# Performance work log

Hardware: AMD Instinct MI355X
Metric: run time of the kernel (lower is better)

Reference implementation:

```python
import jax, jax.numpy as jnp
import numpy as np
from jax import lax

K = 3
K2 = K * K
EPS = 1e-5


def conv3x3(x, w, b=None):
    # x [B,C,H,W], w [O,C,3,3], padding=1, stride=1
    out = lax.conv_general_dilated(x, w, (1, 1), [(1, 1), (1, 1)],
                                   dimension_numbers=('NCHW', 'OIHW', 'NCHW'))
    if b is not None:
        out = out + b[None, :, None, None]
    return out


def deform_conv(x, w_off, b_off, w_mod, b_mod, w):
    # DCNv2-style deformable conv, k=3, stride=1, pad=1, dilation=1, no bias.
    B, C, H, W = x.shape
    O = w.shape[0]
    off = conv3x3(x, w_off, b_off).reshape(B, K2, 2, H, W)   # (dy,dx) per tap
    mod = 2.0 * jax.nn.sigmoid(conv3x3(x, w_mod, b_mod))      # [B,9,H,W]
    dy, dx = off[:, :, 0], off[:, :, 1]

    ky = (jnp.arange(K) - 1).astype(x.dtype)
    base_y = jnp.repeat(ky, K)   # [9]
    base_x = jnp.tile(ky, K)     # [9]
    ii = jnp.arange(H, dtype=x.dtype)[:, None]
    jj = jnp.arange(W, dtype=x.dtype)[None, :]
    py = ii[None, None] + base_y[None, :, None, None] + dy   # [B,9,H,W]
    px = jj[None, None] + base_x[None, :, None, None] + dx

    def sample(xb, pyb, pxb):
        # xb [C,H,W]; pyb/pxb [9,H,W] -> [C,9,H,W], bilinear w/ zero pad
        y0 = jnp.floor(pyb)
        x0 = jnp.floor(pxb)
        wy = pyb - y0
        wx = pxb - x0
        flat = xb.reshape(C, -1)
        acc = jnp.zeros((C, K2, H, W), xb.dtype)
        for yc, xc, wt in ((y0, x0, (1 - wy) * (1 - wx)),
                           (y0, x0 + 1, (1 - wy) * wx),
                           (y0 + 1, x0, wy * (1 - wx)),
                           (y0 + 1, x0 + 1, wy * wx)):
            yi = yc.astype(jnp.int32)
            xi = xc.astype(jnp.int32)
            valid = (yi >= 0) & (yi < H) & (xi >= 0) & (xi < W)
            idx = (jnp.clip(yi, 0, H - 1) * W + jnp.clip(xi, 0, W - 1)).reshape(-1)
            g = jnp.take(flat, idx, axis=1).reshape(C, K2, H, W)
            acc = acc + g * (wt * valid)[None]
        return acc

    patches = jax.vmap(sample)(x, py, px)          # [B,C,9,H,W]
    patches = patches * mod[:, None]               # modulated
    return jnp.einsum('bckhw,ock->bohw', patches, w.reshape(O, C, K2))


def bn_relu(x):
    # BatchNorm2d(affine=False), train-mode batch stats, biased variance
    mean = jnp.mean(x, axis=(0, 2, 3), keepdims=True)
    var = jnp.mean(jnp.square(x - mean), axis=(0, 2, 3), keepdims=True)
    return jax.nn.relu((x - mean) * lax.rsqrt(var + EPS))


def maxpool2(x):
    return lax.reduce_window(x, -jnp.inf, lax.max, (1, 1, 2, 2), (1, 1, 2, 2), 'VALID')


def setup_inputs() -> dict:
    key = jax.random.key(0)
    ks = jax.random.split(key, 11)
    B, Cin, Cout, H, W = 4, 64, 128, 128, 128
    std1 = 1.0 / np.sqrt(Cin * K2)
    std2 = 1.0 / np.sqrt(Cout * K2)
    return {
        'x': jax.random.normal(ks[0], (B, Cin, H, W), jnp.float32),
        'w_off1': jax.random.normal(ks[1], (2 * K2, Cin, K, K), jnp.float32) * 0.01,
        'b_off1': jax.random.normal(ks[2], (2 * K2,), jnp.float32) * 0.01,
        'w_mod1': jax.random.normal(ks[3], (K2, Cin, K, K), jnp.float32) * 0.01,
        'b_mod1': jnp.zeros((K2,), jnp.float32),
        'w1': jax.random.normal(ks[4], (Cout, Cin, K, K), jnp.float32) * std1,
        'w_off2': jax.random.normal(ks[5], (2 * K2, Cout, K, K), jnp.float32) * 0.01,
        'b_off2': jax.random.normal(ks[6], (2 * K2,), jnp.float32) * 0.01,
        'w_mod2': jax.random.normal(ks[7], (K2, Cout, K, K), jnp.float32) * 0.01,
        'b_mod2': jnp.zeros((K2,), jnp.float32),
        'w2': jax.random.normal(ks[8], (Cout, Cout, K, K), jnp.float32) * std2,
    }


def reference(x, w_off1, b_off1, w_mod1, b_mod1, w1,
              w_off2, b_off2, w_mod2, b_mod2, w2):
    h = bn_relu(deform_conv(x, w_off1, b_off1, w_mod1, b_mod1, w1))
    h = bn_relu(deform_conv(h, w_off2, b_off2, w_mod2, b_mod2, w2))
    return maxpool2(h)
```

## Files before the change

kernel.cpp:

```cpp
#include <hip/hip_runtime.h>
#include <math.h>

#define HH 128
#define WW 128
#define HWSZ 16384

typedef __attribute__((ext_vector_type(8))) _Float16 h8;
typedef __attribute__((ext_vector_type(2))) _Float16 h2;
typedef __attribute__((ext_vector_type(4))) float f32x4;
typedef __attribute__((ext_vector_type(2))) float f32x2;
typedef unsigned short ushort;

__device__ __forceinline__ ushort f2h(float f) {
    _Float16 h = (_Float16)f;
    ushort u;
    __builtin_memcpy(&u, &h, 2);
    return u;
}
__device__ __forceinline__ unsigned f2h2(float lo, float hi) {
    h2 r;
    r.x = (_Float16)lo;
    r.y = (_Float16)hi;
    unsigned u;
    __builtin_memcpy(&u, &r, 4);
    return u;
}
__device__ __forceinline__ f32x2 unpk_h2(unsigned u) {
    h2 h;
    __builtin_memcpy(&h, &u, 4);
    return (f32x2){(float)h.x, (float)h.y};
}

__global__ __launch_bounds__(256) void prep_weights(
    const float* __restrict__ w1, const float* __restrict__ w2,
    const float* __restrict__ w_off1, const float* __restrict__ w_mod1,
    const float* __restrict__ w_off2, const float* __restrict__ w_mod2,
    ushort* __restrict__ Wt1, ushort* __restrict__ Wt2,
    ushort* __restrict__ Wo1, ushort* __restrict__ Wo2) {
    int bid = blockIdx.x, tid = threadIdx.x;
    if (bid < 336) {
        int i = bid * 256 + tid;
        int o = i / 672, kq = i % 672;
        int k = kq / 72, c = kq % 72;
        float v = (k < 9 && c < 64) ? w1[(o * 64 + c) * 9 + k] : 0.f;
        Wt1[i] = f2h(v);
    } else if (bid < 960) {
        int i = (bid - 336) * 256 + tid;
        int o = i / 1248, kq = i % 1248;
        int k = kq / 136, c = kq % 136;
        float v = (k < 9 && c < 128) ? w2[(o * 128 + c) * 9 + k] : 0.f;
        Wt2[i] = f2h(v);
    } else if (bid < 1032) {
        int i = (bid - 960) * 256 + tid;
        int o = i / 576, kap = i % 576;
        int k = kap / 64, c = kap % 64;
        float v = 0.f;
        if (o < 18) v = w_off1[(o * 64 + c) * 9 + k];
        else if (o < 27) v = w_mod1[((o - 18) * 64 + c) * 9 + k];
        Wo1[i] = f2h(v);
    } else {
        int i = (bid - 1032) * 256 + tid;
        int o = i / 1152, kap = i % 1152;
        int k = kap / 128, c = kap % 128;
        float v = 0.f;
        if (o < 18) v = w_off2[(o * 128 + c) * 9 + k];
        else if (o < 27) v = w_mod2[((o - 18) * 128 + c) * 9 + k];
        Wo2[i] = f2h(v);
    }
}

template <int C>
__global__ __launch_bounds__(256) void nhwc_cvt(const float* __restrict__ xin,
                                                unsigned* __restrict__ xout) {
    __shared__ float tile[64][C + 1];
    const int m0 = blockIdx.x * 64;
    const int b = m0 >> 14;
    const int hw0 = m0 & 16383;
    const int t = threadIdx.x;
    const int pr = t & 63, cr = t >> 6;
#pragma unroll
    for (int it = 0; it < C / 4; ++it) {
        int c = it * 4 + cr;
        tile[pr][c] = xin[(((size_t)(b * C + c)) << 14) + hw0 + pr];
    }
    __syncthreads();
    constexpr int CH = C / 2;
#pragma unroll
    for (int it = 0; it < 64 * CH / 256; ++it) {
        int slot = it * 256 + t;
        int p = slot / CH, cc = slot % CH;
        xout[(size_t)(m0 + p) * CH + cc] =
            f2h2(tile[p][2 * cc], tile[p][2 * cc + 1]);
    }
}

__global__ __launch_bounds__(256) void bn_apply_ew(
    const unsigned* __restrict__ xin, const float* __restrict__ praw,
    unsigned* __restrict__ xout) {
    __shared__ float lstats[256];
    if (threadIdx.x < 128) {
        int c = threadIdx.x;
        float s = 0.f, q = 0.f;
#pragma unroll
        for (int r = 0; r < 8; ++r) {
            s += praw[r * 256 + c];
            q += praw[r * 256 + 128 + c];
        }
        float mean = s / 65536.f;
        float var = q / 65536.f - mean * mean;
        lstats[c] = mean;
        lstats[128 + c] = rsqrtf(var + 1e-5f);
    }
    __syncthreads();
    int i = blockIdx.x * 256 + threadIdx.x;
    uint4 v = ((const uint4*)xin)[i];
    int c0 = ((i * 4) & 63) * 2;
    unsigned ov[4];
    unsigned in[4] = {v.x, v.y, v.z, v.w};
#pragma unroll
    for (int d = 0; d < 4; ++d) {
        int c = c0 + 2 * d;
        f32x2 f = unpk_h2(in[d]);
        float a = fmaxf(0.f, (f.x - lstats[c]) * lstats[128 + c]);
        float b2 = fmaxf(0.f, (f.y - lstats[c + 1]) * lstats[128 + c + 1]);
        ov[d] = f2h2(a, b2);
    }
    ((uint4*)xout)[i] = uint4{ov[0], ov[1], ov[2], ov[3]};
}

template <int C>
__global__ __launch_bounds__(256) void offmod_nhwc(
    const ushort* __restrict__ xh, const ushort* __restrict__ wt,
    const float* __restrict__ b_off, const float* __restrict__ b_mod,
    float* __restrict__ dyb, float* __restrict__ dxb, float* __restrict__ mob,
    float* __restrict__ praw) {
    constexpr int K = C * 9;
    if (blockIdx.x < 8) praw[blockIdx.x * 256 + threadIdx.x] = 0.f;
    const int m0 = blockIdx.x * 64;
    const int b = m0 >> 14;
    const int hw0 = m0 & 16383;
    const int h = hw0 >> 7;
    const int w0 = hw0 & 127;
    const int tid = threadIdx.x;
    const int lane = tid & 63, wv = tid >> 6;
    const int n16 = lane & 15, quad = lane >> 4;
    const int p = wv * 16 + n16;
    const int w = w0 + p;

    int tbase[9];
    bool tval[9];
#pragma unroll
    for (int k = 0; k < 9; ++k) {
        int yy = h + k / 3 - 1, xx = w + k % 3 - 1;
        tval[k] = ((unsigned)yy < 128u) && ((unsigned)xx < 128u);
        int cy = min(max(yy, 0), 127), cx = min(max(xx, 0), 127);
        tbase[k] = ((b << 14) + (cy << 7) + cx) * C + quad * 8;
    }

    f32x4 acc[2];
    acc[0] = (f32x4){0.f, 0.f, 0.f, 0.f};
    acc[1] = (f32x4){0.f, 0.f, 0.f, 0.f};

    const ushort* b0p = wt + (size_t)n16 * K + quad * 8;
    const ushort* b1p = wt + (size_t)(16 + n16) * K + quad * 8;

#pragma unroll
    for (int s = 0; s < K / 32; ++s) {
        const int k = (s * 32) / C;
        const int c0 = (s * 32) % C;
        h8 a = {0, 0, 0, 0, 0, 0, 0, 0};
        if (tval[k]) a = *(const h8*)(xh + (size_t)tbase[k] + c0);
        const h8 bv0 = *(const h8*)(b0p + s * 32);
        const h8 bv1 = *(const h8*)(b1p + s * 32);
        acc[0] = __builtin_amdgcn_mfma_f32_16x16x32_f16(a, bv0, acc[0], 0, 0, 0);
        acc[1] = __builtin_amdgcn_mfma_f32_16x16x32_f16(a, bv1, acc[1], 0, 0, 0);
    }

    __shared__ float sm[32 * 65];
#pragma unroll
    for (int nt = 0; nt < 2; ++nt) {
        int n = nt * 16 + n16;
        int pb = wv * 16 + quad * 4;
#pragma unroll
        for (int r = 0; r < 4; ++r) sm[n * 65 + pb + r] = acc[nt][r];
    }
    __syncthreads();
    {
        int n = tid >> 3, i8 = tid & 7;
        if (n < 27) {
            const float* sp = sm + n * 65 + i8 * 8;
            int px = hw0 + i8 * 8;
            if (n < 18) {
                int k = n >> 1;
                float bias = b_off[n];
                float* dst =
                    ((n & 1) ? dxb : dyb) + (((size_t)(b * 9 + k)) << 14) + px;
#pragma unroll
                for (int j = 0; j < 8; j += 4) {
                    float4 v = make_float4(sp[j] + bias, sp[j + 1] + bias,
                                           sp[j + 2] + bias, sp[j + 3] + bias);
                    *(float4*)(dst + j) = v;
                }
            } else {
                float bias = b_mod[n - 18];
                float* dst = mob + (((size_t)(b * 9 + (n - 18))) << 14) + px;
#pragma unroll
                for (int j = 0; j < 8; j += 4) {
                    float4 v;
                    v.x = 2.f / (1.f + expf(-(sp[j] + bias)));
                    v.y = 2.f / (1.f + expf(-(sp[j + 1] + bias)));
                    v.z = 2.f / (1.f + expf(-(sp[j + 2] + bias)));
                    v.w = 2.f / (1.f + expf(-(sp[j + 3] + bias)));
                    *(float4*)(dst + j) = v;
                }
            }
        }
    }
}

template <int C>
__global__ __launch_bounds__(256, 4) void deform_mfma3(
    const ushort* __restrict__ xh, const float* __restrict__ dyb,
    const float* __restrict__ dxb, const float* __restrict__ mob,
    const ushort* __restrict__ wt, unsigned* __restrict__ xout,
    float* __restrict__ praw) {
    constexpr int PIX = 64;
    constexpr int NCH = C / 8;
    constexpr int NCC = C / 8;
    constexpr int NIT = PIX * NCC / 256;
    constexpr int HNIT = NIT / 2;
    constexpr int SH = (C / 32) / 2 > 0 ? (C / 32) / 2 : 1;
    constexpr int CPW = C + 8;
    constexpr int KP = ((9 * CPW + 31) / 32) * 32;
    constexpr int ABUF = PIX * C;
    constexpr int LOOPB = 2 * ABUF * 2 + PIX * 9 * 4 + PIX * 9 * 8;
    constexpr int EPIB = 128 * (PIX + 1) * 4;
    constexpr int SMEMB = LOOPB > EPIB ? LOOPB : EPIB;

    __shared__ __align__(16) char smem_raw[SMEMB];
    ushort* abuf0 = (ushort*)smem_raw;
    ushort* abuf1 = abuf0 + ABUF;
    int* tbl = (int*)(abuf0 + 2 * ABUF);
    unsigned* twl = (unsigned*)(smem_raw + 2 * ABUF * 2 + PIX * 9 * 4);

    const int bid = (blockIdx.x & 7) * (gridDim.x >> 3) + (blockIdx.x >> 3);
    const int m0 = bid * PIX;
    const int b = m0 >> 14;
    const int hw0 = m0 & 16383;
    const int h = hw0 >> 7, w0 = hw0 & 127;
    const int tid = threadIdx.x;
    const int lane = tid & 63, wv = tid >> 6;
    const int n16 = lane & 15, quad = lane >> 4;
    const int xr = n16 & (NCH - 1);

    for (int r = tid; r < PIX * 9; r += 256) {
        int p = r & (PIX - 1), k = r >> 6;
        int oi = ((b * 9 + k) << 14) + hw0 + p;
        float py = (float)(h + k / 3 - 1) + dyb[oi];
        float px = (float)(w0 + p + k % 3 - 1) + dxb[oi];
        float mv = mob[oi];
        float y0f = floorf(py), x0f = floorf(px);
        float wy = py - y0f, wx = px - x0f;
        int y0 = (int)y0f, x0 = (int)x0f;
        int y1 = y0 + 1, x1 = x0 + 1;
        float f00 = (1.f - wy) * (1.f - wx) *
                    (((unsigned)y0 < 128u && (unsigned)x0 < 128u) ? mv : 0.f);
        float f01 = (1.f - wy) * wx *
                    (((unsigned)y0 < 128u && (unsigned)x1 < 128u) ? mv : 0.f);
        float f10 = wy * (1.f - wx) *
                    (((unsigned)y1 < 128u && (unsigned)x0 < 128u) ? mv : 0.f);
        float f11 = wy * wx *
                    (((unsigned)y1 < 128u && (unsigned)x1 < 128u) ? mv : 0.f);
        int cy0 = min(max(y0, 0), 127), cy1 = min(max(y1, 0), 127);
        int cx0 = min(max(x0, 0), 127), cx1 = min(max(x1, 0), 127);
        int base00 = (((b << 14) + (cy0 << 7) + cx0)) * C;
        int flags = ((cy1 != cy0) ? 2 : 0) | ((cx1 != cx0) ? 1 : 0);
        int s = p * 9 + k;
        tbl[s] = base00 | flags;
        twl[2 * s] = f2h2(f00, f01);
        twl[2 * s + 1] = f2h2(f10, f11);
    }
    __syncthreads();

    auto issue_loads = [&](int kc, int it0, uint4 (&q)[HNIT][4],
                           uint2 (&fw)[HNIT]) {
#pragma unroll
        for (int j = 0; j < HNIT; ++j) {
            int e = (it0 + j) * 256 + tid;
            int p = e / NCC, cc = e % NCC;
            int s = p * 9 + kc;
            int ent = tbl[s];
            fw[j] = *(const uint2*)&twl[2 * s];
            int base = ent & ~3;
            int dxo = (ent & 1) ? C : 0;
            int dyo = (ent & 2) ? (C << 7) : 0;
            const ushort* pp = xh + (size_t)base + cc * 8;
            q[j][0] = *(const uint4*)(pp);
            q[j][1] = *(const uint4*)(pp + dxo);
            q[j][2] = *(const uint4*)(pp + dyo);
            q[j][3] = *(const uint4*)(pp + dyo + dxo);
        }
    };
    auto interp_write = [&](ushort* dst, int it0, uint4 (&q)[HNIT][4],
                            uint2 (&fw)[HNIT]) {
#pragma unroll
        for (int j = 0; j < HNIT; ++j) {
            int e = (it0 + j) * 256 + tid;
            int p = e / NCC, cc = e % NCC;
            h2 w01, w23;
            __builtin_memcpy(&w01, &fw[j].x, 4);
            __builtin_memcpy(&w23, &fw[j].y, 4);
            h8 F0 = {w01.x, w01.x, w01.x, w01.x, w01.x, w01.x, w01.x, w01.x};
            h8 F1 = {w01.y, w01.y, w01.y, w01.y, w01.y, w01.y, w01.y, w01.y};
            h8 F2 = {w23.x, w23.x, w23.x, w23.x, w23.x, w23.x, w23.x, w23.x};
            h8 F3 = {w23.y, w23.y, w23.y, w23.y, w23.y, w23.y, w23.y, w23.y};
            h8 a0, a1, a2, a3;
            __builtin_memcpy(&a0, &q[j][0], 16);
            __builtin_memcpy(&a1, &q[j][1], 16);
            __builtin_memcpy(&a2, &q[j][2], 16);
            __builtin_memcpy(&a3, &q[j][3], 16);
            h8 v = a0 * F0 + a1 * F1 + a2 * F2 + a3 * F3;
            uint4 ov;
            __builtin_memcpy(&ov, &v, 16);
            int ccs = cc ^ (p & (NCH - 1));
            *(uint4*)&dst[p * C + ccs * 8] = ov;
        }
    };

    f32x4 acc[4][2];
#pragma unroll
    for (int mt = 0; mt < 4; ++mt)
#pragma unroll
        for (int nt = 0; nt < 2; ++nt) acc[mt][nt] = (f32x4){0.f, 0.f, 0.f, 0.f};

    const ushort* bbase[2];
#pragma unroll
    for (int nt = 0; nt < 2; ++nt)
        bbase[nt] = wt + (size_t)(wv * 32 + nt * 16 + n16) * KP + quad * 8;

    auto mfma_run = [&](const ushort* ab, int kc, int s0, int s1) {
#pragma unroll
        for (int s = s0; s < s1; ++s) {
            h8 av[4], bv[2];
            int ch = (s * 4 + quad) ^ xr;
#pragma unroll
            for (int mt = 0; mt < 4; ++mt)
                av[mt] = *(const h8*)(ab + (mt * 16 + n16) * C + ch * 8);
#pragma unroll
            for (int nt = 0; nt < 2; ++nt)
                bv[nt] = *(const h8*)(bbase[nt] + kc * CPW + s * 32);
#pragma unroll
            for (int mt = 0; mt < 4; ++mt)
#pragma unroll
                for (int nt = 0; nt < 2; ++nt)
                    acc[mt][nt] = __builtin_amdgcn_mfma_f32_16x16x32_f16(
                        av[mt], bv[nt], acc[mt][nt], 0, 0, 0);
        }
    };

    {
        uint4 q[HNIT][4];
        uint2 fw[HNIT];
        issue_loads(0, 0, q, fw);
        interp_write(abuf0, 0, q, fw);
        issue_loads(0, HNIT, q, fw);
        interp_write(abuf0, HNIT, q, fw);
    }
    __syncthreads();

#pragma unroll 1
    for (int kc = 0; kc < 9; ++kc) {
        const ushort* ab = (kc & 1) ? abuf1 : abuf0;
        ushort* dst = (kc & 1) ? abuf0 : abuf1;
        uint4 q[HNIT][4];
        uint2 fw[HNIT];
        if (kc < 8) issue_loads(kc + 1, 0, q, fw);
        __builtin_amdgcn_s_setprio(1);
        mfma_run(ab, kc, 0, SH);
        __builtin_amdgcn_s_setprio(0);
        if (kc < 8) {
            interp_write(dst, 0, q, fw);
            issue_loads(kc + 1, HNIT, q, fw);
        }
        __builtin_amdgcn_s_setprio(1);
        mfma_run(ab, kc, SH, C / 32);
        __builtin_amdgcn_s_setprio(0);
        if (kc < 8) interp_write(dst, HNIT, q, fw);
        __syncthreads();
    }

    float* sm = (float*)smem_raw;
    constexpr int SROW = PIX + 1;
#pragma unroll
    for (int mt = 0; mt < 4; ++mt)
#pragma unroll
        for (int nt = 0; nt < 2; ++nt) {
            int o = wv * 32 + nt * 16 + n16;
            int mb = mt * 16 + quad * 4;
#pragma unroll
            for (int r = 0; r < 4; ++r) sm[o * SROW + mb + r] = acc[mt][nt][r];
        }
    __syncthreads();
    {
        int o = tid >> 1, half = tid & 1;
        const float* sp = sm + o * SROW + half * 32;
        float s = 0.f, qq = 0.f;
#pragma unroll
        for (int i = 0; i < 32; i += 4) {
            float4 v = make_float4(sp[i], sp[i + 1], sp[i + 2], sp[i + 3]);
            s += v.x + v.y + v.z + v.w;
            qq += v.x * v.x + v.y * v.y + v.z * v.z + v.w * v.w;
        }
        s += __shfl_down(s, 1, 64);
        qq += __shfl_down(qq, 1, 64);
        if (half == 0) {
            float* pr = praw + (blockIdx.x & 7) * 256;
            atomicAdd(&pr[o], s);
            atomicAdd(&pr[128 + o], qq);
        }
    }
    {
        int p = tid >> 2, cc4 = tid & 3;
        unsigned ov[16];
#pragma unroll
        for (int j = 0; j < 16; ++j) {
            int c = cc4 * 32 + 2 * j;
            ov[j] = f2h2(sm[c * SROW + p], sm[(c + 1) * SROW + p]);
        }
        uint4* dst = (uint4*)(xout + ((size_t)(m0 + p)) * 64 + cc4 * 16);
        dst[0] = uint4{ov[0], ov[1], ov[2], ov[3]};
        dst[1] = uint4{ov[4], ov[5], ov[6], ov[7]};
        dst[2] = uint4{ov[8], ov[9], ov[10], ov[11]};
        dst[3] = uint4{ov[12], ov[13], ov[14], ov[15]};
    }
}

template <int C>
__global__ __launch_bounds__(256, 4) void deform_mfma3p(
    const ushort* __restrict__ xh, const float* __restrict__ dyb,
    const float* __restrict__ dxb, const float* __restrict__ mob,
    const ushort* __restrict__ wt, float* __restrict__ pout,
    float* __restrict__ praw) {
    constexpr int PIX = 64;
    constexpr int NCH = C / 8;
    constexpr int NCC = C / 8;
    constexpr int NIT = PIX * NCC / 256;
    constexpr int HNIT = NIT / 2;
    constexpr int SH = (C / 32) / 2 > 0 ? (C / 32) / 2 : 1;
    constexpr int CPW = C + 8;
    constexpr int KP = ((9 * CPW + 31) / 32) * 32;
    constexpr int ABUF = PIX * C;
    constexpr int LOOPB = 2 * ABUF * 2 + PIX * 9 * 4 + PIX * 9 * 8;
    constexpr int EPIB = 128 * (PIX + 1) * 4;
    constexpr int SMEMB = LOOPB > EPIB ? LOOPB : EPIB;

    __shared__ __align__(16) char smem_raw[SMEMB];
    ushort* abuf0 = (ushort*)smem_raw;
    ushort* abuf1 = abuf0 + ABUF;
    int* tbl = (int*)(abuf0 + 2 * ABUF);
    unsigned* twl = (unsigned*)(smem_raw + 2 * ABUF * 2 + PIX * 9 * 4);

    const int bid = (blockIdx.x & 7) * (gridDim.x >> 3) + (blockIdx.x >> 3);
    const int b = bid >> 8;
    const int rp = (bid >> 2) & 63;
    const int g = bid & 3;
    const int tid = threadIdx.x;
    const int lane = tid & 63, wv = tid >> 6;
    const int n16 = lane & 15, quad = lane >> 4;
    const int xr = n16 & (NCH - 1);

    for (int r = tid; r < PIX * 9; r += 256) {
        int p = r & (PIX - 1), k = r >> 6;
        int row = 2 * rp + (p >> 5), col = g * 32 + (p & 31);
        int oi = ((b * 9 + k) << 14) + (row << 7) + col;
        float py = (float)(row + k / 3 - 1) + dyb[oi];
        float px = (float)(col + k % 3 - 1) + dxb[oi];
        float mv = mob[oi];
        float y0f = floorf(py), x0f = floorf(px);
        float wy = py - y0f, wx = px - x0f;
        int y0 = (int)y0f, x0 = (int)x0f;
        int y1 = y0 + 1, x1 = x0 + 1;
        float f00 = (1.f - wy) * (1.f - wx) *
                    (((unsigned)y0 < 128u && (unsigned)x0 < 128u) ? mv : 0.f);
        float f01 = (1.f - wy) * wx *
                    (((unsigned)y0 < 128u && (unsigned)x1 < 128u) ? mv : 0.f);
        float f10 = wy * (1.f - wx) *
                    (((unsigned)y1 < 128u && (unsigned)x0 < 128u) ? mv : 0.f);
        float f11 = wy * wx *
                    (((unsigned)y1 < 128u && (unsigned)x1 < 128u) ? mv : 0.f);
        int cy0 = min(max(y0, 0), 127), cy1 = min(max(y1, 0), 127);
        int cx0 = min(max(x0, 0), 127), cx1 = min(max(x1, 0), 127);
        int base00 = (((b << 14) + (cy0 << 7) + cx0)) * C;
        int flags = ((cy1 != cy0) ? 2 : 0) | ((cx1 != cx0) ? 1 : 0);
        int s = p * 9 + k;
        tbl[s] = base00 | flags;
        twl[2 * s] = f2h2(f00, f01);
        twl[2 * s + 1] = f2h2(f10, f11);
    }
    __syncthreads();

    auto issue_loads = [&](int kc, int it0, uint4 (&q)[HNIT][4],
                           uint2 (&fw)[HNIT]) {
#pragma unroll
        for (int j = 0; j < HNIT; ++j) {
            int e = (it0 + j) * 256 + tid;
            int p = e / NCC, cc = e % NCC;
            int s = p * 9 + kc;
            int ent = tbl[s];
            fw[j] = *(const uint2*)&twl[2 * s];
            int base = ent & ~3;
            int dxo = (ent & 1) ? C : 0;
            int dyo = (ent & 2) ? (C << 7) : 0;
            const ushort* pp = xh + (size_t)base + cc * 8;
            q[j][0] = *(const uint4*)(pp);
            q[j][1] = *(const uint4*)(pp + dxo);
            q[j][2] = *(const uint4*)(pp + dyo);
            q[j][3] = *(const uint4*)(pp + dyo + dxo);
        }
    };
    auto interp_write = [&](ushort* dst, int it0, uint4 (&q)[HNIT][4],
                            uint2 (&fw)[HNIT]) {
#pragma unroll
        for (int j = 0; j < HNIT; ++j) {
            int e = (it0 + j) * 256 + tid;
            int p = e / NCC, cc = e % NCC;
            h2 w01, w23;
            __builtin_memcpy(&w01, &fw[j].x, 4);
            __builtin_memcpy(&w23, &fw[j].y, 4);
            h8 F0 = {w01.x, w01.x, w01.x, w01.x, w01.x, w01.x, w01.x, w01.x};
            h8 F1 = {w01.y, w01.y, w01.y, w01.y, w01.y, w01.y, w01.y, w01.y};
            h8 F2 = {w23.x, w23.x, w23.x, w23.x, w23.x, w23.x, w23.x, w23.x};
            h8 F3 = {w23.y, w23.y, w23.y, w23.y, w23.y, w23.y, w23.y, w23.y};
            h8 a0, a1, a2, a3;
            __builtin_memcpy(&a0, &q[j][0], 16);
            __builtin_memcpy(&a1, &q[j][1], 16);
            __builtin_memcpy(&a2, &q[j][2], 16);
            __builtin_memcpy(&a3, &q[j][3], 16);
            h8 v = a0 * F0 + a1 * F1 + a2 * F2 + a3 * F3;
            uint4 ov;
            __builtin_memcpy(&ov, &v, 16);
            int ccs = cc ^ (p & (NCH - 1));
            *(uint4*)&dst[p * C + ccs * 8] = ov;
        }
    };

    f32x4 acc[4][2];
#pragma unroll
    for (int mt = 0; mt < 4; ++mt)
#pragma unroll
        for (int nt = 0; nt < 2; ++nt) acc[mt][nt] = (f32x4){0.f, 0.f, 0.f, 0.f};

    const ushort* bbase[2];
#pragma unroll
    for (int nt = 0; nt < 2; ++nt)
        bbase[nt] = wt + (size_t)(wv * 32 + nt * 16 + n16) * KP + quad * 8;

    auto mfma_run = [&](const ushort* ab, int kc, int s0, int s1) {
#pragma unroll
        for (int s = s0; s < s1; ++s) {
            h8 av[4], bv[2];
            int ch = (s * 4 + quad) ^ xr;
#pragma unroll
            for (int mt = 0; mt < 4; ++mt)
                av[mt] = *(const h8*)(ab + (mt * 16 + n16) * C + ch * 8);
#pragma unroll
            for (int nt = 0; nt < 2; ++nt)
                bv[nt] = *(const h8*)(bbase[nt] + kc * CPW + s * 32);
#pragma unroll
            for (int mt = 0; mt < 4; ++mt)
#pragma unroll
                for (int nt = 0; nt < 2; ++nt)
                    acc[mt][nt] = __builtin_amdgcn_mfma_f32_16x16x32_f16(
                        av[mt], bv[nt], acc[mt][nt], 0, 0, 0);
        }
    };

    {
        uint4 q[HNIT][4];
        uint2 fw[HNIT];
        issue_loads(0, 0, q, fw);
        interp_write(abuf0, 0, q, fw);
        issue_loads(0, HNIT, q, fw);
        interp_write(abuf0, HNIT, q, fw);
    }
    __syncthreads();

#pragma unroll 1
    for (int kc = 0; kc < 9; ++kc) {
        const ushort* ab = (kc & 1) ? abuf1 : abuf0;
        ushort* dst = (kc & 1) ? abuf0 : abuf1;
        uint4 q[HNIT][4];
        uint2 fw[HNIT];
        if (kc < 8) issue_loads(kc + 1, 0, q, fw);
        __builtin_amdgcn_s_setprio(1);
        mfma_run(ab, kc, 0, SH);
        __builtin_amdgcn_s_setprio(0);
        if (kc < 8) {
            interp_write(dst, 0, q, fw);
            issue_loads(kc + 1, HNIT, q, fw);
        }
        __builtin_amdgcn_s_setprio(1);
        mfma_run(ab, kc, SH, C / 32);
        __builtin_amdgcn_s_setprio(0);
        if (kc < 8) interp_write(dst, HNIT, q, fw);
        __syncthreads();
    }

    float* sm = (float*)smem_raw;
    constexpr int SROW = PIX + 1;
#pragma unroll
    for (int mt = 0; mt < 4; ++mt)
#pragma unroll
        for (int nt = 0; nt < 2; ++nt) {
            int o = wv * 32 + nt * 16 + n16;
            int mb = mt * 16 + quad * 4;
#pragma unroll
            for (int r = 0; r < 4; ++r) sm[o * SROW + mb + r] = acc[mt][nt][r];
        }
    __syncthreads();
    {
        int o = tid >> 1, half = tid & 1;
        const float* so = sm + o * SROW;
        const float* sp = so + half * 32;
        float s = 0.f, qq = 0.f;
#pragma unroll
        for (int i = 0; i < 32; i += 4) {
            float4 v = make_float4(sp[i], sp[i + 1], sp[i + 2], sp[i + 3]);
            s += v.x + v.y + v.z + v.w;
            qq += v.x * v.x + v.y * v.y + v.z * v.z + v.w * v.w;
        }
        s += __shfl_down(s, 1, 64);
        qq += __shfl_down(qq, 1, 64);
        if (half == 0) {
            float* pr = praw + (blockIdx.x & 7) * 256;
            atomicAdd(&pr[o], s);
            atomicAdd(&pr[128 + o], qq);
        }
        float4 pv0, pv1;
#pragma unroll
        for (int i = 0; i < 8; ++i) {
            int pc = half * 8 + i;
            float m0v = fmaxf(so[2 * pc], so[2 * pc + 1]);
            float m1v = fmaxf(so[32 + 2 * pc], so[32 + 2 * pc + 1]);
            float m = fmaxf(m0v, m1v);
            if (i < 4) ((float*)&pv0)[i] = m;
            else ((float*)&pv1)[i - 4] = m;
        }
        float* dp = pout + (((size_t)(b * 128 + o)) << 12) + rp * 64 + g * 16 +
                    half * 8;
        *(float4*)(dp) = pv0;
        *(float4*)(dp + 4) = pv1;
    }
}

__global__ __launch_bounds__(256) void pool_norm(const float* __restrict__ pout,
                                                 const float* __restrict__ praw,
                                                 float* __restrict__ out) {
    __shared__ float lstats[256];
    if (threadIdx.x < 128) {
        int c = threadIdx.x;
        float s = 0.f, q = 0.f;
#pragma unroll
        for (int r = 0; r < 8; ++r) {
            s += praw[r * 256 + c];
            q += praw[r * 256 + 128 + c];
        }
        float mean = s / 65536.f;
        float var = q / 65536.f - mean * mean;
        lstats[c] = mean;
        lstats[128 + c] = rsqrtf(var + 1e-5f);
    }
    __syncthreads();
    int i = blockIdx.x * 256 + threadIdx.x;
    int c = (i >> 10) & 127;
    float mean = lstats[c], rstd = lstats[128 + c];
    float4 v = ((const float4*)pout)[i];
    v.x = fmaxf(0.f, (v.x - mean) * rstd);
    v.y = fmaxf(0.f, (v.y - mean) * rstd);
    v.z = fmaxf(0.f, (v.z - mean) * rstd);
    v.w = fmaxf(0.f, (v.w - mean) * rstd);
    ((float4*)out)[i] = v;
}

extern "C" void kernel_launch(void* const* d_in, const int* in_sizes, int n_in,
                              void* d_out, int out_size, void* d_ws,
                              size_t ws_size, hipStream_t stream) {
    (void)in_sizes;
    (void)n_in;
    (void)out_size;
    (void)ws_size;
    const float* x = (const float*)d_in[0];
    const float* w_off1 = (const float*)d_in[1];
    const float* b_off1 = (const float*)d_in[2];
    const float* w_mod1 = (const float*)d_in[3];
    const float* b_mod1 = (const float*)d_in[4];
    const float* w1 = (const float*)d_in[5];
    const float* w_off2 = (const float*)d_in[6];
    const float* b_off2 = (const float*)d_in[7];
    const float* w_mod2 = (const float*)d_in[8];
    const float* b_mod2 = (const float*)d_in[9];
    const float* w2 = (const float*)d_in[10];
    float* out = (float*)d_out;
    float* ws = (float*)d_ws;

    ushort* Wt1 = (ushort*)ws;
    ushort* Wt2 = (ushort*)(ws + 43008);
    ushort* Wo1 = (ushort*)(ws + 43008 + 79872);
    ushort* Wo2 = (ushort*)(ws + 43008 + 79872 + 16384);
    float* dyb = ws + 172032;
    float* dxb = dyb + 589824;
    float* mob = dxb + 589824;
    float* hbuf = mob + 589824;
    float* xhf = hbuf + 8388608;
    float* h1hf = xhf + 2097152;
    float* praw = h1hf + 4194304;
    ushort* xh = (ushort*)xhf;
    ushort* h1h = (ushort*)h1hf;

    prep_weights<<<1176, 256, 0, stream>>>(w1, w2, w_off1, w_mod1, w_off2,
                                           w_mod2, Wt1, Wt2, Wo1, Wo2);

    nhwc_cvt<64><<<1024, 256, 0, stream>>>(x, (unsigned*)xh);
    offmod_nhwc<64><<<1024, 256, 0, stream>>>(xh, Wo1, b_off1, b_mod1, dyb, dxb,
                                              mob, praw);
    deform_mfma3<64><<<1024, 256, 0, stream>>>(xh, dyb, dxb, mob, Wt1,
                                               (unsigned*)hbuf, praw);
    bn_apply_ew<<<4096, 256, 0, stream>>>((const unsigned*)hbuf, praw,
                                          (unsigned*)h1h);

    offmod_nhwc<128><<<1024, 256, 0, stream>>>(h1h, Wo2, b_off2, b_mod2, dyb,
                                               dxb, mob, praw);
    deform_mfma3p<128><<<1024, 256, 0, stream>>>(h1h, dyb, dxb, mob, Wt2, hbuf,
                                                 praw);
    pool_norm<<<2048, 256, 0, stream>>>(hbuf, praw, out);
}
```

Before: 250.1 us.

## Fuse first BatchNorm+ReLU into second-layer offset and deform kernels

```diff
diff --git a/kernel.cpp b/kernel.cpp
--- a/kernel.cpp
+++ b/kernel.cpp
@@ -29,6 +29,19 @@
     h2 h;
     __builtin_memcpy(&h, &u, 4);
     return (f32x2){(float)h.x, (float)h.y};
+}
+__device__ __forceinline__ h8 nrelu8(h8 a, h8 R, h8 N) {
+    h8 t = a * R + N;
+#if __has_builtin(__builtin_elementwise_max)
+    h8 z = {};
+    return __builtin_elementwise_max(t, z);
+#else
+    h8 r;
+#pragma unroll
+    for (int i = 0; i < 8; ++i)
+        r[i] = t[i] > (_Float16)0 ? t[i] : (_Float16)0;
+    return r;
+#endif
 }
 
 __global__ __launch_bounds__(256) void prep_weights(
@@ -94,48 +107,15 @@
     }
 }
 
-__global__ __launch_bounds__(256) void bn_apply_ew(
-    const unsigned* __restrict__ xin, const float* __restrict__ praw,
-    unsigned* __restrict__ xout) {
-    __shared__ float lstats[256];
-    if (threadIdx.x < 128) {
-        int c = threadIdx.x;
-        float s = 0.f, q = 0.f;
-#pragma unroll
-        for (int r = 0; r < 8; ++r) {
-            s += praw[r * 256 + c];
-            q += praw[r * 256 + 128 + c];
-        }
-        float mean = s / 65536.f;
-        float var = q / 65536.f - mean * mean;
-        lstats[c] = mean;
-        lstats[128 + c] = rsqrtf(var + 1e-5f);
-    }
-    __syncthreads();
-    int i = blockIdx.x * 256 + threadIdx.x;
-    uint4 v = ((const uint4*)xin)[i];
-    int c0 = ((i * 4) & 63) * 2;
-    unsigned ov[4];
-    unsigned in[4] = {v.x, v.y, v.z, v.w};
-#pragma unroll
-    for (int d = 0; d < 4; ++d) {
-        int c = c0 + 2 * d;
-        f32x2 f = unpk_h2(in[d]);
-        float a = fmaxf(0.f, (f.x - lstats[c]) * lstats[128 + c]);
-        float b2 = fmaxf(0.f, (f.y - lstats[c + 1]) * lstats[128 + c + 1]);
-        ov[d] = f2h2(a, b2);
-    }
-    ((uint4*)xout)[i] = uint4{ov[0], ov[1], ov[2], ov[3]};
-}
-
-template <int C>
+template <int C, bool NORM>
 __global__ __launch_bounds__(256) void offmod_nhwc(
     const ushort* __restrict__ xh, const ushort* __restrict__ wt,
     const float* __restrict__ b_off, const float* __restrict__ b_mod,
     float* __restrict__ dyb, float* __restrict__ dxb, float* __restrict__ mob,
-    float* __restrict__ praw) {
+    float* __restrict__ praw_out, const float* __restrict__ pr_in) {
     constexpr int K = C * 9;
-    if (blockIdx.x < 8) praw[blockIdx.x * 256 + threadIdx.x] = 0.f;
+    __shared__ unsigned cstat[128];
+    if (blockIdx.x < 8) praw_out[blockIdx.x * 256 + threadIdx.x] = 0.f;
     const int m0 = blockIdx.x * 64;
     const int b = m0 >> 14;
     const int hw0 = m0 & 16383;
@@ -147,6 +127,36 @@
     const int p = wv * 16 + n16;
     const int w = w0 + p;
 
+    if (NORM) {
+        if (tid < 64) {
+            int c0i = 2 * tid, c1i = 2 * tid + 1;
+            float s0 = 0.f, q0 = 0.f, s1 = 0.f, q1 = 0.f;
+#pragma unroll
+            for (int r = 0; r < 8; ++r) {
+                s0 += pr_in[r * 256 + c0i];
+                q0 += pr_in[r * 256 + 128 + c0i];
+                s1 += pr_in[r * 256 + c1i];
+                q1 += pr_in[r * 256 + 128 + c1i];
+            }
+            float m0v = s0 / 65536.f, m1v = s1 / 65536.f;
+            float r0 = rsqrtf(q0 / 65536.f - m0v * m0v + 1e-5f);
+            float r1 = rsqrtf(q1 / 65536.f - m1v * m1v + 1e-5f);
+            cstat[tid] = f2h2(r0, r1);
+            cstat[64 + tid] = f2h2(-m0v * r0, -m1v * r1);
+        }
+        __syncthreads();
+    }
+
+    h8 Rv[4], Nv[4];
+    if (NORM) {
+#pragma unroll
+        for (int si = 0; si < 4; ++si) {
+            int db = si * 16 + quad * 4;
+            Rv[si] = *(const h8*)&cstat[db];
+            Nv[si] = *(const h8*)&cstat[64 + db];
+        }
+    }
+
     int tbase[9];
     bool tval[9];
 #pragma unroll
@@ -169,7 +179,13 @@
         const int k = (s * 32) / C;
         const int c0 = (s * 32) % C;
         h8 a = {0, 0, 0, 0, 0, 0, 0, 0};
-        if (tval[k]) a = *(const h8*)(xh + (size_t)tbase[k] + c0);
+        if (tval[k]) {
+            a = *(const h8*)(xh + (size_t)tbase[k] + c0);
+            if (NORM) {
+                const int si = s & ((C / 32) - 1);
+                a = nrelu8(a, Rv[si], Nv[si]);
+            }
+        }
         const h8 bv0 = *(const h8*)(b0p + s * 32);
         const h8 bv1 = *(const h8*)(b1p + s * 32);
         acc[0] = __builtin_amdgcn_mfma_f32_16x16x32_f16(a, bv0, acc[0], 0, 0, 0);
@@ -440,7 +456,7 @@
     const ushort* __restrict__ xh, const float* __restrict__ dyb,
     const float* __restrict__ dxb, const float* __restrict__ mob,
     const ushort* __restrict__ wt, float* __restrict__ pout,
-    float* __restrict__ praw) {
+    float* __restrict__ praw, const float* __restrict__ pr_in) {
     constexpr int PIX = 64;
     constexpr int NCH = C / 8;
     constexpr int NCC = C / 8;
@@ -452,13 +468,14 @@
     constexpr int ABUF = PIX * C;
     constexpr int LOOPB = 2 * ABUF * 2 + PIX * 9 * 4 + PIX * 9 * 8;
     constexpr int EPIB = 128 * (PIX + 1) * 4;
-    constexpr int SMEMB = LOOPB > EPIB ? LOOPB : EPIB;
+    constexpr int SMEMB = (LOOPB > EPIB ? LOOPB : EPIB) + 512;
 
     __shared__ __align__(16) char smem_raw[SMEMB];
     ushort* abuf0 = (ushort*)smem_raw;
     ushort* abuf1 = abuf0 + ABUF;
     int* tbl = (int*)(abuf0 + 2 * ABUF);
     unsigned* twl = (unsigned*)(smem_raw + 2 * ABUF * 2 + PIX * 9 * 4);
+    unsigned* cst = (unsigned*)(smem_raw + (SMEMB - 512));
 
     const int bid = (blockIdx.x & 7) * (gridDim.x >> 3) + (blockIdx.x >> 3);
     const int b = bid >> 8;
@@ -468,6 +485,23 @@
     const int lane = tid & 63, wv = tid >> 6;
     const int n16 = lane & 15, quad = lane >> 4;
     const int xr = n16 & (NCH - 1);
+
+    if (tid < 64) {
+        int c0i = 2 * tid, c1i = 2 * tid + 1;
+        float s0 = 0.f, q0 = 0.f, s1 = 0.f, q1 = 0.f;
+#pragma unroll
+        for (int r = 0; r < 8; ++r) {
+            s0 += pr_in[r * 256 + c0i];
+            q0 += pr_in[r * 256 + 128 + c0i];
+            s1 += pr_in[r * 256 + c1i];
+            q1 += pr_in[r * 256 + 128 + c1i];
+        }
+        float m0v = s0 / 65536.f, m1v = s1 / 65536.f;
+        float r0 = rsqrtf(q0 / 65536.f - m0v * m0v + 1e-5f);
+        float r1 = rsqrtf(q1 / 65536.f - m1v * m1v + 1e-5f);
+        cst[tid] = f2h2(r0, r1);
+        cst[64 + tid] = f2h2(-m0v * r0, -m1v * r1);
+    }
 
     for (int r = tid; r < PIX * 9; r += 256) {
         int p = r & (PIX - 1), k = r >> 6;
@@ -499,6 +533,10 @@
     }
     __syncthreads();
 
+    const int ccf = tid & (NCC - 1);
+    const h8 Rv = *(const h8*)&cst[ccf * 4];
+    const h8 Nv = *(const h8*)&cst[64 + ccf * 4];
+
     auto issue_loads = [&](int kc, int it0, uint4 (&q)[HNIT][4],
                            uint2 (&fw)[HNIT]) {
 #pragma unroll
@@ -536,6 +574,10 @@
             __builtin_memcpy(&a1, &q[j][1], 16);
             __builtin_memcpy(&a2, &q[j][2], 16);
             __builtin_memcpy(&a3, &q[j][3], 16);
+            a0 = nrelu8(a0, Rv, Nv);
+            a1 = nrelu8(a1, Rv, Nv);
+            a2 = nrelu8(a2, Rv, Nv);
+            a3 = nrelu8(a3, Rv, Nv);
             h8 v = a0 * F0 + a1 * F1 + a2 * F2 + a3 * F3;
             uint4 ov;
             __builtin_memcpy(&ov, &v, 16);
@@ -713,24 +755,23 @@
     float* hbuf = mob + 589824;
     float* xhf = hbuf + 8388608;
     float* h1hf = xhf + 2097152;
-    float* praw = h1hf + 4194304;
+    float* praw1 = h1hf + 4194304;
+    float* praw2 = praw1 + 2048;
     ushort* xh = (ushort*)xhf;
-    ushort* h1h = (ushort*)h1hf;
+    ushort* hb = (ushort*)hbuf;
 
     prep_weights<<<1176, 256, 0, stream>>>(w1, w2, w_off1, w_mod1, w_off2,
                                            w_mod2, Wt1, Wt2, Wo1, Wo2);
 
     nhwc_cvt<64><<<1024, 256, 0, stream>>>(x, (unsigned*)xh);
-    offmod_nhwc<64><<<1024, 256, 0, stream>>>(xh, Wo1, b_off1, b_mod1, dyb, dxb,
-                                              mob, praw);
+    offmod_nhwc<64, false><<<1024, 256, 0, stream>>>(
+        xh, Wo1, b_off1, b_mod1, dyb, dxb, mob, praw1, praw1);
     deform_mfma3<64><<<1024, 256, 0, stream>>>(xh, dyb, dxb, mob, Wt1,
-                                               (unsigned*)hbuf, praw);
-    bn_apply_ew<<<4096, 256, 0, stream>>>((const unsigned*)hbuf, praw,
-                                          (unsigned*)h1h);
-
-    offmod_nhwc<128><<<1024, 256, 0, stream>>>(h1h, Wo2, b_off2, b_mod2, dyb,
-                                               dxb, mob, praw);
-    deform_mfma3p<128><<<1024, 256, 0, stream>>>(h1h, dyb, dxb, mob, Wt2, hbuf,
-                                                 praw);
-    pool_norm<<<2048, 256, 0, stream>>>(hbuf, praw, out);
-}
+                                               (unsigned*)hbuf, praw1);
+
+    offmod_nhwc<128, true><<<1024, 256, 0, stream>>>(
+        hb, Wo2, b_off2, b_mod2, dyb, dxb, mob, praw2, praw1);
+    deform_mfma3p<128><<<1024, 256, 0, stream>>>(hb, dyb, dxb, mob, Wt2, h1hf,
+                                                 praw2, praw1);
+    pool_norm<<<2048, 256, 0, stream>>>(h1hf, praw2, out);
+}
```

After: 250.6 us. Within noise of the previous version (+0.2%).
